# Kernel optimization log

Hardware: AMD Instinct MI355X
Metric: run time of the kernel (lower is better)

The kernel has to match this reference:

```python
import jax, jax.numpy as jnp
import numpy as np

N = 100000      # num nodes == input_dim (featureless RGCN)
S = 50          # support (num relations)
B = 30          # num_bases
OUT = 16        # output_dim
E = 20000       # edges per relation


def setup_inputs() -> dict:
    key = jax.random.key(0)
    k1, k2, k3, k4, k5, k6 = jax.random.split(key, 6)
    features = jax.random.normal(k1, (N, 1), dtype=jnp.float32)
    src = jax.random.randint(k2, (S, E), 0, N, dtype=jnp.int32)
    dst = jax.random.randint(k3, (S, E), 0, N, dtype=jnp.int32)
    vals = jax.random.uniform(k4, (S, E), dtype=jnp.float32)
    # learned params (xavier-ish scale)
    W = jax.random.normal(k5, (N * B, OUT), dtype=jnp.float32) * (2.0 / (N * B + OUT)) ** 0.5
    W_comp = jax.random.normal(k6, (S, B), dtype=jnp.float32) * (2.0 / (S + B)) ** 0.5
    return {"features": features, "src": src, "dst": dst, "vals": vals, "W": W, "W_comp": W_comp}


def reference(features, src, dst, vals, W, W_comp):
    n = features.shape[0]  # == N (featureless: input_dim == num_nodes)
    # Basis decomposition, exactly as torch:
    # V = W_comp @ W.reshape(B, N, OUT).permute(1, 0, 2)  -> [N, S, OUT]
    Wb = W.reshape(B, n, OUT).transpose(1, 0, 2)          # [N, B, OUT]
    V = jnp.einsum('sb,nbo->nso', W_comp, Wb)             # [N, S, OUT]
    # torch reshape (support*input_dim, OUT): row k = node*S + rel (node-major)
    V2 = V.reshape(S * n, OUT)                            # [S*N, OUT]
    # supports is block-concat sparse [N, S*N], column = rel*N + node (relation-major)
    # output = supports @ V2: for edge (i=src, j=dst) in relation r:
    #   out[i] += val * V2[r*N + j]
    gather_idx = (jnp.arange(S, dtype=src.dtype)[:, None] * n + dst).reshape(-1)  # [S*E]
    msgs = V2[gather_idx] * vals.reshape(-1, 1)           # [S*E, OUT]
    out = jax.ops.segment_sum(msgs, src.reshape(-1), num_segments=n)  # [N, OUT]
    # featureless dropout scaling: tmp = dropout(ones(N)); p=0 -> identity
    return jax.nn.relu(out)
```

## Files before the change

### kernel.cpp

```cpp
#include <hip/hip_runtime.h>

constexpr int S_REL = 50;
constexpr int B_BASES = 30;
constexpr int OUT_DIM = 16;
constexpr int TILE_N = 32;

__global__ __launch_bounds__(128) void build_v2_tiled(
    const float4* __restrict__ W4, const float* __restrict__ Wcomp,
    float4* __restrict__ V24, int N) {
    __shared__ float scw[S_REL * B_BASES];
    const int t = threadIdx.x;
    const int nodeBase = blockIdx.x * TILE_N;
    const int nf4 = N * 4;

    for (int i = t; i < S_REL * B_BASES; i += 128) scw[i] = Wcomp[i];

    float4 f[B_BASES];
    const int off = nodeBase * 4 + t;
#pragma unroll
    for (int b = 0; b < B_BASES; ++b)
        f[b] = (off < nf4) ? W4[(size_t)b * nf4 + off]
                           : make_float4(0.f, 0.f, 0.f, 0.f);
    __syncthreads();

    const int nl = t >> 2;
    const int o4 = t & 3;
    const int node = nodeBase + nl;
    if (node >= N) return;

    for (int rel = 0; rel < S_REL; ++rel) {
        const float* c = &scw[rel * B_BASES];
        float4 a = make_float4(0.f, 0.f, 0.f, 0.f);
#pragma unroll
        for (int b = 0; b < B_BASES; ++b) {
            float cb = c[b];
            a.x = fmaf(cb, f[b].x, a.x);
            a.y = fmaf(cb, f[b].y, a.y);
            a.z = fmaf(cb, f[b].z, a.z);
            a.w = fmaf(cb, f[b].w, a.w);
        }
        V24[((size_t)node * S_REL + rel) * 4 + o4] = a;
    }
}

__global__ __launch_bounds__(256) void hist_kernel(
    const int* __restrict__ src, unsigned* __restrict__ cnt, int nEdges) {
    int i = blockIdx.x * blockDim.x + threadIdx.x;
    int stride = gridDim.x * blockDim.x;
    for (; i < nEdges; i += stride) atomicAdd(&cnt[src[i]], 1u);
}

__global__ __launch_bounds__(1024) void scanA_kernel(
    const unsigned* __restrict__ cnt, unsigned* __restrict__ offs,
    unsigned* __restrict__ bsum, int N) {
    __shared__ unsigned s[1024];
    const int t = threadIdx.x;
    const int i = blockIdx.x * 1024 + t;
    unsigned x = (i < N) ? cnt[i] : 0u;
    s[t] = x;
    __syncthreads();
    for (int d = 1; d < 1024; d <<= 1) {
        unsigned v = (t >= d) ? s[t - d] : 0u;
        __syncthreads();
        s[t] += v;
        __syncthreads();
    }
    if (i < N) offs[i] = s[t] - x;
    if (t == 1023) bsum[blockIdx.x] = s[1023];
}

__global__ __launch_bounds__(64) void scanB_kernel(
    unsigned* __restrict__ bsum, unsigned* __restrict__ bofs, int nb) {
    if (threadIdx.x == 0) {
        unsigned run = 0;
        for (int j = 0; j < nb; ++j) { unsigned x = bsum[j]; bofs[j] = run; run += x; }
    }
}

__global__ __launch_bounds__(1024) void scanC_kernel(
    unsigned* __restrict__ offs, unsigned* __restrict__ cur,
    const unsigned* __restrict__ bofs, int N, int nEdges) {
    const int i = blockIdx.x * 1024 + threadIdx.x;
    if (i < N) {
        unsigned o = offs[i] + bofs[i >> 10];
        offs[i] = o;
        cur[i] = o;
    }
    if (i == 0) offs[N] = (unsigned)nEdges;
}

__global__ __launch_bounds__(256) void consume_kernel(
    const int* __restrict__ src, const int* __restrict__ dst,
    const float* __restrict__ vals, const float4* __restrict__ V24,
    float4* __restrict__ M4, unsigned* __restrict__ cur,
    int N, int E, int nEdges) {
    int t = blockIdx.x * blockDim.x + threadIdx.x;
    int e = t >> 2;
    int q = t & 3;
    if (e >= nEdges) return;
    int r = e / E;
    int d = dst[e];
    int s = src[e];
    float v = vals[e];
    int k = r * N + d;
    float4 g = V24[(size_t)k * 4 + q];
    float4 m = make_float4(v * g.x, v * g.y, v * g.z, v * g.w);
    unsigned pos = 0;
    if (q == 0) pos = atomicAdd(&cur[s], 1u);
    pos = __shfl(pos, 0, 4);
    M4[(size_t)pos * 4 + q] = m;
}

__global__ __launch_bounds__(256) void reduce_kernel(
    const float4* __restrict__ M4, const unsigned* __restrict__ offs,
    float4* __restrict__ out4, int N) {
    int t = blockIdx.x * blockDim.x + threadIdx.x;
    int n = t >> 2;
    int q = t & 3;
    if (n >= N) return;
    unsigned b = offs[n];
    unsigned e = offs[n + 1];
    float4 a = make_float4(0.f, 0.f, 0.f, 0.f);
    for (unsigned p = b; p < e; ++p) {
        float4 m = M4[(size_t)p * 4 + q];
        a.x += m.x; a.y += m.y; a.z += m.z; a.w += m.w;
    }
    out4[(size_t)n * 4 + q] = make_float4(fmaxf(a.x, 0.f), fmaxf(a.y, 0.f),
                                          fmaxf(a.z, 0.f), fmaxf(a.w, 0.f));
}

constexpr int NXCD = 8;
constexpr int EDGES_PER_BLOCK = 64;

__global__ __launch_bounds__(256) void relu_inplace_kernel(float4* __restrict__ p, int n4) {
    int i = blockIdx.x * blockDim.x + threadIdx.x;
    int stride = gridDim.x * blockDim.x;
    for (; i < n4; i += stride) {
        float4 v = p[i];
        v.x = fmaxf(v.x, 0.f); v.y = fmaxf(v.y, 0.f);
        v.z = fmaxf(v.z, 0.f); v.w = fmaxf(v.w, 0.f);
        p[i] = v;
    }
}

__global__ __launch_bounds__(256) void rgcn_edge_atomic_kernel(
    const int* __restrict__ src, const int* __restrict__ dst,
    const float* __restrict__ vals, const float* __restrict__ W,
    const float* __restrict__ Wcomp, float* __restrict__ out,
    int N, int E, int nEdges, int chunksPerXcd, int nChunks) {
    __shared__ float wc[S_REL * B_BASES];
    for (int i = threadIdx.x; i < S_REL * B_BASES; i += blockDim.x) wc[i] = Wcomp[i];
    __syncthreads();
    const int x = blockIdx.x % NXCD;
    const int j = blockIdx.x / NXCD;
    const int chunk = x * chunksPerXcd + j;
    if (chunk >= nChunks) return;
    const int edge = chunk * EDGES_PER_BLOCK + (threadIdx.x >> 2);
    const int o4 = (threadIdx.x & 3) * 4;
    if (edge >= nEdges) return;
    const int r = edge / E;
    const int d = dst[edge];
    const int s = src[edge];
    const float v = vals[edge];
    const int k = r * N + d;
    const int node = k / S_REL;
    const int rel = k - node * S_REL;
    const float* wp = W + (size_t)node * OUT_DIM + o4;
    const size_t bstride = (size_t)N * OUT_DIM;
    const float* wcr = wc + rel * B_BASES;
    float4 acc = make_float4(0.f, 0.f, 0.f, 0.f);
#pragma unroll
    for (int b = 0; b < B_BASES; ++b) {
        float4 w4 = *reinterpret_cast<const float4*>(wp + (size_t)b * bstride);
        float c = wcr[b];
        acc.x = fmaf(c, w4.x, acc.x); acc.y = fmaf(c, w4.y, acc.y);
        acc.z = fmaf(c, w4.z, acc.z); acc.w = fmaf(c, w4.w, acc.w);
    }
    float* op = out + (size_t)s * OUT_DIM + o4;
    atomicAdd(op + 0, v * acc.x); atomicAdd(op + 1, v * acc.y);
    atomicAdd(op + 2, v * acc.z); atomicAdd(op + 3, v * acc.w);
}

extern "C" void kernel_launch(void* const* d_in, const int* in_sizes, int n_in,
                              void* d_out, int out_size, void* d_ws, size_t ws_size,
                              hipStream_t stream) {
    const int* src = (const int*)d_in[1];
    const int* dst = (const int*)d_in[2];
    const float* vals = (const float*)d_in[3];
    const float* W = (const float*)d_in[4];
    const float* Wcomp = (const float*)d_in[5];

    const int N = in_sizes[0];
    const int nEdges = in_sizes[1];
    const int E = nEdges / S_REL;

    const int nbScan = (N + 1023) / 1024;
    const size_t v2Bytes = (size_t)S_REL * N * OUT_DIM * sizeof(float);
    const size_t msgBytes = (size_t)nEdges * OUT_DIM * sizeof(float);
    const size_t intBytes = ((size_t)3 * N + 1 + 2 * nbScan) * sizeof(unsigned);
    const size_t needed = v2Bytes + msgBytes + intBytes;

    if (ws_size < needed) {
        float* out = (float*)d_out;
        hipMemsetAsync(d_out, 0, (size_t)out_size * sizeof(float), stream);
        const int nChunks = (nEdges + EDGES_PER_BLOCK - 1) / EDGES_PER_BLOCK;
        const int chunksPerXcd = (nChunks + NXCD - 1) / NXCD;
        rgcn_edge_atomic_kernel<<<chunksPerXcd * NXCD, 256, 0, stream>>>(
            src, dst, vals, W, Wcomp, out, N, E, nEdges, chunksPerXcd, nChunks);
        const int n4 = out_size / 4;
        int zb = (n4 + 255) / 256;
        relu_inplace_kernel<<<(zb < 2048 ? zb : 2048), 256, 0, stream>>>((float4*)out, n4);
        return;
    }

    float4* V24 = (float4*)d_ws;
    float4* M4 = (float4*)((char*)d_ws + v2Bytes);
    unsigned* cnt = (unsigned*)((char*)d_ws + v2Bytes + msgBytes);
    unsigned* offs = cnt + N;
    unsigned* cur = offs + N + 1;
    unsigned* bsum = cur + N;
    unsigned* bofs = bsum + nbScan;

    const int bblocks = (N + TILE_N - 1) / TILE_N;
    build_v2_tiled<<<bblocks, 128, 0, stream>>>((const float4*)W, Wcomp, V24, N);

    hipMemsetAsync(cnt, 0, (size_t)N * sizeof(unsigned), stream);
    int hb = (nEdges + 255) / 256;
    hist_kernel<<<(hb < 2048 ? hb : 2048), 256, 0, stream>>>(src, cnt, nEdges);
    scanA_kernel<<<nbScan, 1024, 0, stream>>>(cnt, offs, bsum, N);
    scanB_kernel<<<1, 64, 0, stream>>>(bsum, bofs, nbScan);
    scanC_kernel<<<nbScan, 1024, 0, stream>>>(offs, cur, bofs, N, nEdges);

    const long long cthreads = (long long)nEdges * 4;
    consume_kernel<<<(int)((cthreads + 255) / 256), 256, 0, stream>>>(
        src, dst, vals, V24, M4, cur, N, E, nEdges);

    const int rblocks = (N * 4 + 255) / 256;
    reduce_kernel<<<rblocks, 256, 0, stream>>>(M4, offs, (float4*)d_out, N);
}
```

Measured before the change: 586.6 us.

## Replace dense V2 precompute with per-edge basis combination over node-sorted edges

Removes the build_v2_tiled kernel, which wrote the full S*N*16 V2 table, and instead computes each edge's 16-wide message on the fly from the 30 basis rows of W. Edges are first counting-sorted by their W node index into a packed payload, so neighbouring edges reuse the same W rows through cache. The messages are then written into src-sorted slots and reduced as before. This avoids writing and reading the large V2 table, at the cost of extra histogram, scan and scatter passes and 30 W loads per edge.

```diff
diff --git a/kernel.cpp b/kernel.cpp
--- a/kernel.cpp
+++ b/kernel.cpp
@@ -3,60 +3,30 @@
 constexpr int S_REL = 50;
 constexpr int B_BASES = 30;
 constexpr int OUT_DIM = 16;
-constexpr int TILE_N = 32;
-
-__global__ __launch_bounds__(128) void build_v2_tiled(
-    const float4* __restrict__ W4, const float* __restrict__ Wcomp,
-    float4* __restrict__ V24, int N) {
-    __shared__ float scw[S_REL * B_BASES];
-    const int t = threadIdx.x;
-    const int nodeBase = blockIdx.x * TILE_N;
-    const int nf4 = N * 4;
-
-    for (int i = t; i < S_REL * B_BASES; i += 128) scw[i] = Wcomp[i];
-
-    float4 f[B_BASES];
-    const int off = nodeBase * 4 + t;
-#pragma unroll
-    for (int b = 0; b < B_BASES; ++b)
-        f[b] = (off < nf4) ? W4[(size_t)b * nf4 + off]
-                           : make_float4(0.f, 0.f, 0.f, 0.f);
-    __syncthreads();
-
-    const int nl = t >> 2;
-    const int o4 = t & 3;
-    const int node = nodeBase + nl;
-    if (node >= N) return;
-
-    for (int rel = 0; rel < S_REL; ++rel) {
-        const float* c = &scw[rel * B_BASES];
-        float4 a = make_float4(0.f, 0.f, 0.f, 0.f);
-#pragma unroll
-        for (int b = 0; b < B_BASES; ++b) {
-            float cb = c[b];
-            a.x = fmaf(cb, f[b].x, a.x);
-            a.y = fmaf(cb, f[b].y, a.y);
-            a.z = fmaf(cb, f[b].z, a.z);
-            a.w = fmaf(cb, f[b].w, a.w);
-        }
-        V24[((size_t)node * S_REL + rel) * 4 + o4] = a;
-    }
-}
-
-__global__ __launch_bounds__(256) void hist_kernel(
-    const int* __restrict__ src, unsigned* __restrict__ cnt, int nEdges) {
+constexpr int NXCD = 8;
+constexpr int EDGES_PER_BLOCK = 64;
+
+__global__ __launch_bounds__(256) void hist2_kernel(
+    const int* __restrict__ src, const int* __restrict__ dst,
+    unsigned* __restrict__ cntNode, unsigned* __restrict__ cntSrc,
+    int N, int E, int nEdges) {
     int i = blockIdx.x * blockDim.x + threadIdx.x;
     int stride = gridDim.x * blockDim.x;
-    for (; i < nEdges; i += stride) atomicAdd(&cnt[src[i]], 1u);
+    for (; i < nEdges; i += stride) {
+        int r = i / E;
+        int node = (r * N + dst[i]) / S_REL;
+        atomicAdd(&cntNode[node], 1u);
+        atomicAdd(&cntSrc[src[i]], 1u);
+    }
 }
 
 __global__ __launch_bounds__(1024) void scanA_kernel(
     const unsigned* __restrict__ cnt, unsigned* __restrict__ offs,
-    unsigned* __restrict__ bsum, int N) {
+    unsigned* __restrict__ bsum, int NB) {
     __shared__ unsigned s[1024];
     const int t = threadIdx.x;
     const int i = blockIdx.x * 1024 + t;
-    unsigned x = (i < N) ? cnt[i] : 0u;
+    unsigned x = (i < NB) ? cnt[i] : 0u;
     s[t] = x;
     __syncthreads();
     for (int d = 1; d < 1024; d <<= 1) {
@@ -65,7 +35,7 @@
         s[t] += v;
         __syncthreads();
     }
-    if (i < N) offs[i] = s[t] - x;
+    if (i < NB) offs[i] = s[t] - x;
     if (t == 1023) bsum[blockIdx.x] = s[1023];
 }
 
@@ -79,36 +49,77 @@
 
 __global__ __launch_bounds__(1024) void scanC_kernel(
     unsigned* __restrict__ offs, unsigned* __restrict__ cur,
-    const unsigned* __restrict__ bofs, int N, int nEdges) {
+    const unsigned* __restrict__ bofs, int NB, int total) {
     const int i = blockIdx.x * 1024 + threadIdx.x;
-    if (i < N) {
+    if (i < NB) {
         unsigned o = offs[i] + bofs[i >> 10];
         offs[i] = o;
         cur[i] = o;
     }
-    if (i == 0) offs[N] = (unsigned)nEdges;
-}
-
-__global__ __launch_bounds__(256) void consume_kernel(
+    if (i == 0) offs[NB] = (unsigned)total;
+}
+
+__global__ __launch_bounds__(256) void scatter_kernel(
     const int* __restrict__ src, const int* __restrict__ dst,
-    const float* __restrict__ vals, const float4* __restrict__ V24,
-    float4* __restrict__ M4, unsigned* __restrict__ cur,
-    int N, int E, int nEdges) {
-    int t = blockIdx.x * blockDim.x + threadIdx.x;
-    int e = t >> 2;
-    int q = t & 3;
+    const float* __restrict__ vals, float4* __restrict__ pay,
+    unsigned* __restrict__ curNode, int N, int E, int nEdges) {
+    int i = blockIdx.x * blockDim.x + threadIdx.x;
+    int stride = gridDim.x * blockDim.x;
+    for (; i < nEdges; i += stride) {
+        int r = i / E;
+        int d = dst[i];
+        int k = r * N + d;
+        int node = k / S_REL;
+        int dmod = k - node * S_REL;
+        unsigned pos = atomicAdd(&curNode[node], 1u);
+        pay[pos] = make_float4(__int_as_float(src[i]), __int_as_float(dmod),
+                               vals[i], __int_as_float(node));
+    }
+}
+
+__global__ __launch_bounds__(256) void edge_sorted_kernel(
+    const float4* __restrict__ pay, const float4* __restrict__ W4,
+    const float* __restrict__ Wcomp, float4* __restrict__ M4,
+    unsigned* __restrict__ curSrc, int N, int nEdges,
+    int chunksPerXcd, int nChunks) {
+    __shared__ float scw[S_REL * B_BASES];
+    for (int i = threadIdx.x; i < S_REL * B_BASES; i += blockDim.x)
+        scw[i] = Wcomp[i];
+    __syncthreads();
+
+    const int x = blockIdx.x % NXCD;
+    const int j = blockIdx.x / NXCD;
+    const int chunk = x * chunksPerXcd + j;
+    if (chunk >= nChunks) return;
+    const int e = chunk * EDGES_PER_BLOCK + (threadIdx.x >> 2);
+    const int q = threadIdx.x & 3;
     if (e >= nEdges) return;
-    int r = e / E;
-    int d = dst[e];
-    int s = src[e];
-    float v = vals[e];
-    int k = r * N + d;
-    float4 g = V24[(size_t)k * 4 + q];
-    float4 m = make_float4(v * g.x, v * g.y, v * g.z, v * g.w);
+
+    float4 p = pay[e];
+    const int s = __float_as_int(p.x);
+    const int dmod = __float_as_int(p.y);
+    const float v = p.z;
+    const int node = __float_as_int(p.w);
+
+    const float4* wp = W4 + (size_t)node * 4 + q;
+    const size_t bstride = (size_t)N * 4;
+    const float* c = &scw[dmod * B_BASES];
+
+    float4 a = make_float4(0.f, 0.f, 0.f, 0.f);
+#pragma unroll
+    for (int b = 0; b < B_BASES; ++b) {
+        float4 w = wp[(size_t)b * bstride];
+        float cb = c[b];
+        a.x = fmaf(cb, w.x, a.x);
+        a.y = fmaf(cb, w.y, a.y);
+        a.z = fmaf(cb, w.z, a.z);
+        a.w = fmaf(cb, w.w, a.w);
+    }
+
     unsigned pos = 0;
-    if (q == 0) pos = atomicAdd(&cur[s], 1u);
+    if (q == 0) pos = atomicAdd(&curSrc[s], 1u);
     pos = __shfl(pos, 0, 4);
-    M4[(size_t)pos * 4 + q] = m;
+    M4[(size_t)pos * 4 + q] = make_float4(v * a.x, v * a.y, v * a.z, v * a.w);
 }
 
 __global__ __launch_bounds__(256) void reduce_kernel(
@@ -128,9 +139,6 @@
     out4[(size_t)n * 4 + q] = make_float4(fmaxf(a.x, 0.f), fmaxf(a.y, 0.f),
                                           fmaxf(a.z, 0.f), fmaxf(a.w, 0.f));
 }
-
-constexpr int NXCD = 8;
-constexpr int EDGES_PER_BLOCK = 64;
 
 __global__ __launch_bounds__(256) void relu_inplace_kernel(float4* __restrict__ p, int n4) {
     int i = blockIdx.x * blockDim.x + threadIdx.x;
@@ -194,18 +202,20 @@
     const int nEdges = in_sizes[1];
     const int E = nEdges / S_REL;
 
-    const int nbScan = (N + 1023) / 1024;
-    const size_t v2Bytes = (size_t)S_REL * N * OUT_DIM * sizeof(float);
-    const size_t msgBytes = (size_t)nEdges * OUT_DIM * sizeof(float);
-    const size_t intBytes = ((size_t)3 * N + 1 + 2 * nbScan) * sizeof(unsigned);
-    const size_t needed = v2Bytes + msgBytes + intBytes;
+    const int nb = (N + 1023) / 1024;
+    const size_t payBytes = (size_t)nEdges * sizeof(float4);
+    const size_t mBytes = (size_t)nEdges * OUT_DIM * sizeof(float);
+    const size_t uints = (size_t)6 * N + 2 + 2 * nb;
+    const size_t needed = payBytes + mBytes + uints * sizeof(unsigned);
+
+    const int nChunks = (nEdges + EDGES_PER_BLOCK - 1) / EDGES_PER_BLOCK;
+    const int chunksPerXcd = (nChunks + NXCD - 1) / NXCD;
+    const int eblocks = chunksPerXcd * NXCD;
 
     if (ws_size < needed) {
         float* out = (float*)d_out;
         hipMemsetAsync(d_out, 0, (size_t)out_size * sizeof(float), stream);
-        const int nChunks = (nEdges + EDGES_PER_BLOCK - 1) / EDGES_PER_BLOCK;
-        const int chunksPerXcd = (nChunks + NXCD - 1) / NXCD;
-        rgcn_edge_atomic_kernel<<<chunksPerXcd * NXCD, 256, 0, stream>>>(
+        rgcn_edge_atomic_kernel<<<eblocks, 256, 0, stream>>>(
             src, dst, vals, W, Wcomp, out, N, E, nEdges, chunksPerXcd, nChunks);
         const int n4 = out_size / 4;
         int zb = (n4 + 255) / 256;
@@ -213,28 +223,36 @@
         return;
     }
 
-    float4* V24 = (float4*)d_ws;
-    float4* M4 = (float4*)((char*)d_ws + v2Bytes);
-    unsigned* cnt = (unsigned*)((char*)d_ws + v2Bytes + msgBytes);
-    unsigned* offs = cnt + N;
-    unsigned* cur = offs + N + 1;
-    unsigned* bsum = cur + N;
-    unsigned* bofs = bsum + nbScan;
-
-    const int bblocks = (N + TILE_N - 1) / TILE_N;
-    build_v2_tiled<<<bblocks, 128, 0, stream>>>((const float4*)W, Wcomp, V24, N);
-
-    hipMemsetAsync(cnt, 0, (size_t)N * sizeof(unsigned), stream);
-    int hb = (nEdges + 255) / 256;
-    hist_kernel<<<(hb < 2048 ? hb : 2048), 256, 0, stream>>>(src, cnt, nEdges);
-    scanA_kernel<<<nbScan, 1024, 0, stream>>>(cnt, offs, bsum, N);
-    scanB_kernel<<<1, 64, 0, stream>>>(bsum, bofs, nbScan);
-    scanC_kernel<<<nbScan, 1024, 0, stream>>>(offs, cur, bofs, N, nEdges);
-
-    const long long cthreads = (long long)nEdges * 4;
-    consume_kernel<<<(int)((cthreads + 255) / 256), 256, 0, stream>>>(
-        src, dst, vals, V24, M4, cur, N, E, nEdges);
+    float4* pay = (float4*)d_ws;
+    float4* M4 = (float4*)((char*)d_ws + payBytes);
+    unsigned* cnt1 = (unsigned*)((char*)d_ws + payBytes + mBytes);
+    unsigned* cnt2 = cnt1 + N;
+    unsigned* offs1 = cnt2 + N;
+    unsigned* cur1 = offs1 + N + 1;
+    unsigned* offs2 = cur1 + N;
+    unsigned* cur2 = offs2 + N + 1;
+    unsigned* bsum = cur2 + N;
+    unsigned* bofs = bsum + nb;
+
+    hipMemsetAsync(cnt1, 0, (size_t)2 * N * sizeof(unsigned), stream);
+
+    int gb = (nEdges + 255) / 256;
+    if (gb > 2048) gb = 2048;
+    hist2_kernel<<<gb, 256, 0, stream>>>(src, dst, cnt1, cnt2, N, E, nEdges);
+
+    scanA_kernel<<<nb, 1024, 0, stream>>>(cnt1, offs1, bsum, N);
+    scanB_kernel<<<1, 64, 0, stream>>>(bsum, bofs, nb);
+    scanC_kernel<<<nb, 1024, 0, stream>>>(offs1, cur1, bofs, N, nEdges);
+
+    scatter_kernel<<<gb, 256, 0, stream>>>(src, dst, vals, pay, cur1, N, E, nEdges);
+
+    scanA_kernel<<<nb, 1024, 0, stream>>>(cnt2, offs2, bsum, N);
+    scanB_kernel<<<1, 64, 0, stream>>>(bsum, bofs, nb);
+    scanC_kernel<<<nb, 1024, 0, stream>>>(offs2, cur2, bofs, N, nEdges);
+
+    edge_sorted_kernel<<<eblocks, 256, 0, stream>>>(
+        pay, (const float4*)W, Wcomp, M4, cur2, N, nEdges, chunksPerXcd, nChunks);
 
     const int rblocks = (N * 4 + 255) / 256;
-    reduce_kernel<<<rblocks, 256, 0, stream>>>(M4, offs, (float4*)d_out, N);
-}
+    reduce_kernel<<<rblocks, 256, 0, stream>>>(M4, offs2, (float4*)d_out, N);
+}
```

New measurement: 584.0 us. Within noise of the previous version (-0.4%).
